# Performance work log

Hardware: AMD Instinct MI355X
Metric: run time of the kernel (lower is better)

## Reference

```python
import jax, jax.numpy as jnp
import numpy as np
from jax import lax

T, B, S = 64, 32, 64
V, E, H = 32000, 512, 512

def _p(key, shape, scale=0.05):
    return (jax.random.normal(key, shape, dtype=jnp.float32) * scale)

def setup_inputs() -> dict:
    key = jax.random.key(0)
    ks = jax.random.split(key, 24)
    inp = {
        'trg': jax.random.randint(ks[0], (T, B), 0, V),
        'encoded_src': jax.random.normal(ks[1], (S, B, 2 * H), dtype=jnp.float32),
        'emb': _p(ks[2], (V, E)),
        # LSTM layer 0: input = E + 2H
        'W_ih0': _p(ks[3], (4 * H, E + 2 * H)), 'W_hh0': _p(ks[4], (4 * H, H)),
        'b_ih0': _p(ks[5], (4 * H,)), 'b_hh0': _p(ks[6], (4 * H,)),
        # LSTM layer 1: input = H
        'W_ih1': _p(ks[7], (4 * H, H)), 'W_hh1': _p(ks[8], (4 * H, H)),
        'b_ih1': _p(ks[9], (4 * H,)), 'b_hh1': _p(ks[10], (4 * H,)),
        # attn_annot: 2H -> H
        'Wa': _p(ks[11], (H, 2 * H)), 'ba': _p(ks[12], (H,)),
        # attn_hidden: H -> H
        'Wh': _p(ks[13], (H, H)), 'bh': _p(ks[14], (H,)),
        # other: H -> 1
        'Wo': _p(ks[15], (1, H)), 'bo': _p(ks[16], (1,)),
        # penult: 3H -> E
        'Wp': _p(ks[17], (E, 3 * H)), 'bp': _p(ks[18], (E,)),
        # out bias (weight tied to emb)
        'b_out': _p(ks[19], (V,)),
    }
    return inp

def _lstm_cell(x, h, c, W_ih, W_hh, b_ih, b_hh):
    # PyTorch gate order: i, f, g, o
    g = x @ W_ih.T + b_ih + h @ W_hh.T + b_hh
    i, f, gg, o = jnp.split(g, 4, axis=-1)
    c_new = jax.nn.sigmoid(f) * c + jax.nn.sigmoid(i) * jnp.tanh(gg)
    h_new = jax.nn.sigmoid(o) * jnp.tanh(c_new)
    return h_new, c_new

def reference(trg, encoded_src, emb, W_ih0, W_hh0, b_ih0, b_hh0,
              W_ih1, W_hh1, b_ih1, b_hh1, Wa, ba, Wh, bh, Wo, bo,
              Wp, bp, b_out):
    trg_emb = emb[trg]                                # [T,B,E]
    annot_scores = encoded_src @ Wa.T + ba            # [S,B,H]
    Hd = W_hh0.shape[1]
    Bd = encoded_src.shape[1]
    h0 = jnp.zeros((2, Bd, Hd), dtype=encoded_src.dtype)
    c0 = jnp.zeros((2, Bd, Hd), dtype=encoded_src.dtype)
    ctx0 = jnp.zeros((Bd, encoded_src.shape[2]), dtype=encoded_src.dtype)

    def step(carry, emb_t):
        h, c, ctx = carry
        x = jnp.concatenate([emb_t, ctx], axis=1)      # [B, E+2H]
        h0n, c0n = _lstm_cell(x,   h[0], c[0], W_ih0, W_hh0, b_ih0, b_hh0)
        h1n, c1n = _lstm_cell(h0n, h[1], c[1], W_ih1, W_hh1, b_ih1, b_hh1)
        out = h1n                                      # [B,H]
        hs = out @ Wh.T + bh                           # [B,H]
        e = jnp.tanh(hs[None] + annot_scores) @ Wo.T + bo   # [S,B,1]
        a = jax.nn.softmax(e, axis=0)[..., 0]          # [S,B]
        ctx_new = jnp.einsum('sb,sbd->bd', a, encoded_src)  # [B,2H]
        stacked = jnp.concatenate([out, ctx_new], axis=1)   # [B,3H]
        return (jnp.stack([h0n, h1n]), jnp.stack([c0n, c1n]), ctx_new), stacked

    (h, c, _), all_scores = lax.scan(step, (h0, c0, ctx0), trg_emb)  # all_scores [T,B,3H]
    pen = all_scores @ Wp.T + bp                       # [T,B,E]
    logits = pen @ emb.T + b_out                       # [T,B,V] (tied weights)
    scores = jax.nn.log_softmax(logits, axis=2)
    return (scores, h, c)
```

## Files before the change

kernel.cpp:

```cpp
#include <hip/hip_runtime.h>


typedef unsigned short u16;
typedef short bf16x8 __attribute__((ext_vector_type(8)));
typedef float f32x4 __attribute__((ext_vector_type(4)));

#define MFMA_BF16(a, b, c) __builtin_amdgcn_mfma_f32_16x16x32_bf16((a), (b), (c), 0, 0, 0)

struct __attribute__((aligned(8))) U16x4 { u16 x, y, z, w; };

__device__ __forceinline__ float b2f(u16 u) {
  unsigned v = ((unsigned)u) << 16; float f; __builtin_memcpy(&f, &v, 4); return f;
}
__device__ __forceinline__ u16 f2b(float f) {
  unsigned u; __builtin_memcpy(&u, &f, 4);
  u = (u + 0x7FFFu + ((u >> 16) & 1u)) >> 16;
  return (u16)u;
}
__device__ __forceinline__ float sigm(float x) { return 1.f / (1.f + __expf(-x)); }
__device__ __forceinline__ float tanh_fast(float x) {
  x = fminf(fmaxf(x, -15.f), 15.f);
  float e = __expf(2.f * x);
  return (e - 1.f) / (e + 1.f);
}

__device__ __forceinline__ bf16x8 bl16(const u16* p) {
  bf16x8 v;
  asm volatile("global_load_dwordx4 %0, %1, off sc1" : "=v"(v) : "v"(p) : "memory");
  return v;
}
__device__ __forceinline__ float blf(const float* p) {
  float v;
  asm volatile("global_load_dword %0, %1, off sc1" : "=v"(v) : "v"(p) : "memory");
  return v;
}
__device__ __forceinline__ u16 blu16(const u16* p) {
  unsigned v;
  asm volatile("global_load_ushort %0, %1, off sc1" : "=v"(v) : "v"(p) : "memory");
  return (u16)v;
}
__device__ __forceinline__ void bs16(u16* p, u16 d) {
  unsigned dd = d;
  asm volatile("global_store_short %0, %1, off sc1" :: "v"(p), "v"(dd) : "memory");
}
__device__ __forceinline__ void bs32u(u16* p, unsigned d) {
  asm volatile("global_store_dword %0, %1, off sc1" :: "v"(p), "v"(d) : "memory");
}
__device__ __forceinline__ void bsf32(float* p, float d) {
  asm volatile("global_store_dword %0, %1, off sc1" :: "v"(p), "v"(d) : "memory");
}
__device__ __forceinline__ bf16x8 cl16(const u16* p) {
  bf16x8 v;
  asm volatile("global_load_dwordx4 %0, %1, off" : "=v"(v) : "v"(p));
  return v;
}
__device__ __forceinline__ void vmwait() {
  asm volatile("s_waitcnt vmcnt(0)" ::: "memory");
  __builtin_amdgcn_sched_barrier(0);
}

__device__ __forceinline__ void seg_f2b4(const float* src, u16* dst, long n4,
                                         int bid, int nb) {
  long i = (long)bid * 256 + threadIdx.x;
  long stride = (long)nb * 256;
  for (; i < n4; i += stride) {
    float4 v = ((const float4*)src)[i];
    U16x4 o; o.x = f2b(v.x); o.y = f2b(v.y); o.z = f2b(v.z); o.w = f2b(v.w);
    ((U16x4*)dst)[i] = o;
  }
}
__device__ __forceinline__ void seg_strided(const float* src, u16* dst,
                                            int rows, int cols4, int sld, int soff,
                                            int dld, int doff, int bid, int nb) {
  int total = rows * cols4;
  for (int i = bid * 256 + threadIdx.x; i < total; i += nb * 256) {
    int r = i / cols4, c4 = i - r * cols4;
    float4 v = *(const float4*)(src + (size_t)r * sld + soff + c4 * 4);
    U16x4 o; o.x = f2b(v.x); o.y = f2b(v.y); o.z = f2b(v.z); o.w = f2b(v.w);
    *(U16x4*)(dst + (size_t)r * dld + doff + c4 * 4) = o;
  }
}

__global__ __launch_bounds__(256) void prep_all(
    const float* __restrict__ emb, const float* __restrict__ enc,
    const float* __restrict__ Wa, const float* __restrict__ Wh,
    const float* __restrict__ Wp, const float* __restrict__ W_ih0,
    const float* __restrict__ W_hh0, const float* __restrict__ W_ih1,
    const float* __restrict__ W_hh1, const int* __restrict__ trg,
    u16* __restrict__ emb_b, u16* __restrict__ enc_b, u16* __restrict__ Wa_b,
    u16* __restrict__ Wh_b, u16* __restrict__ Wp_b, u16* __restrict__ Wemb0_b,
    u16* __restrict__ Wcat0_b, u16* __restrict__ Wcat1_b,
    u16* __restrict__ trgemb_b, u16* __restrict__ enc_bt,
    float* __restrict__ zero_base) {
  const int bx = blockIdx.x;
  if (bx < 32) {
    for (int i = bx * 256 + threadIdx.x; i < 24832; i += 32 * 256) {
      ((float4*)zero_base)[i] = make_float4(0.f, 0.f, 0.f, 0.f);
    }
  } else if (bx < 1056) {
    seg_f2b4(emb, emb_b, 4096000, bx - 32, 1024);
  } else if (bx < 1312) {
    seg_f2b4(enc, enc_b, 524288, bx - 1056, 256);
  } else if (bx < 1376) {
    seg_f2b4(Wa, Wa_b, 131072, bx - 1312, 64);
  } else if (bx < 1408) {
    seg_f2b4(Wh, Wh_b, 65536, bx - 1376, 32);
  } else if (bx < 1536) {
    seg_f2b4(Wp, Wp_b, 196608, bx - 1408, 128);
  } else if (bx < 2048) {
    seg_strided(W_ih0, Wemb0_b, 2048, 128, 1536, 0, 512, 0, bx - 1536, 512);
  } else if (bx < 2560) {
    seg_strided(W_ih0, Wcat0_b, 2048, 256, 1536, 512, 1536, 0, bx - 2048, 512);
  } else if (bx < 3072) {
    seg_strided(W_hh0, Wcat0_b, 2048, 128, 512, 0, 1536, 1024, bx - 2560, 512);
  } else if (bx < 3584) {
    seg_strided(W_ih1, Wcat1_b, 2048, 128, 512, 0, 1024, 0, bx - 3072, 512);
  } else if (bx < 4096) {
    seg_strided(W_hh1, Wcat1_b, 2048, 128, 512, 0, 1024, 512, bx - 3584, 512);
  } else if (bx < 6144) {
    int r = bx - 4096;
    int v = trg[r];
    const float* srow = emb + (size_t)v * 512;
    u16* drow = trgemb_b + (size_t)r * 512;
    for (int e = threadIdx.x; e < 128; e += 256) {
      float4 x = ((const float4*)srow)[e];
      U16x4 o; o.x = f2b(x.x); o.y = f2b(x.y); o.z = f2b(x.z); o.w = f2b(x.w);
      ((U16x4*)drow)[e] = o;
    }
  } else {
    int r = bx - 6144;
    int b = r >> 6, s = r & 63;
    const float* src = enc + (size_t)(s * 32 + b) * 1024;
    u16* dst = enc_bt + (size_t)(b * 64 + s) * 1024;
    int j = threadIdx.x;
    float4 v = ((const float4*)src)[j];
    U16x4 o; o.x = f2b(v.x); o.y = f2b(v.y); o.z = f2b(v.z); o.w = f2b(v.w);
    ((U16x4*)dst)[j] = o;
  }
}

template <int MODE>
__global__ __launch_bounds__(256) void gemm_bt(
    const u16* __restrict__ A, const u16* __restrict__ B,
    float* __restrict__ outF, u16* __restrict__ outB,
    const float* __restrict__ bias0, const float* __restrict__ bias1,
    int N, int K) {
  const int l = threadIdx.x & 63, wv = threadIdx.x >> 6;
  const int m0 = blockIdx.x * 128 + wv * 32;
  const int n0 = blockIdx.y * 64;
  const int kg = ((l >> 4) << 3);
  const u16* Ap0 = A + (size_t)(m0 + (l & 15)) * K + kg;
  const u16* Ap1 = Ap0 + (size_t)16 * K;
  const u16* Bp = B + (size_t)(n0 + (l & 15)) * K + kg;
  f32x4 acc[2][4] = {};
  for (int k0 = 0; k0 < K; k0 += 32) {
    bf16x8 a0 = *(const bf16x8*)(Ap0 + k0);
    bf16x8 a1 = *(const bf16x8*)(Ap1 + k0);
#pragma unroll
    for (int nf = 0; nf < 4; ++nf) {
      bf16x8 bb = *(const bf16x8*)(Bp + (size_t)(nf * 16) * K + k0);
      acc[0][nf] = MFMA_BF16(a0, bb, acc[0][nf]);
      acc[1][nf] = MFMA_BF16(a1, bb, acc[1][nf]);
    }
  }
  float biasv[4];
#pragma unroll
  for (int nf = 0; nf < 4; ++nf) {
    int col = n0 + nf * 16 + (l & 15);
    float bv = bias0 ? bias0[col] : 0.f;
    if (bias1) bv += bias1[col];
    biasv[nf] = bv;
  }
#pragma unroll
  for (int mi = 0; mi < 2; ++mi)
#pragma unroll
    for (int i = 0; i < 4; ++i) {
      int row = m0 + mi * 16 + ((l >> 4) << 2) + i;
#pragma unroll
      for (int nf = 0; nf < 4; ++nf) {
        int col = n0 + nf * 16 + (l & 15);
        float v = acc[mi][nf][i] + biasv[nf];
        if constexpr (MODE == 1) {
          outB[(size_t)row * N + col] = f2b(v);
        } else if constexpr (MODE == 3) {
          int b = row & 31, s = row >> 5;
          outB[(size_t)(b * 64 + s) * 512 + col] = f2b(v);
        } else {
          outF[(size_t)row * N + col] = v;
        }
      }
    }
}

__global__ __launch_bounds__(256) void logits_kernel(
    const u16* __restrict__ A,
    const u16* __restrict__ B,
    const float* __restrict__ bias,
    float* __restrict__ out,
    float* __restrict__ pmax, float* __restrict__ psum) {
  __shared__ float smf[128 * 132];
  const int id = blockIdx.x;
  const int lin = (id & 7) * 500 + (id >> 3);
  const int mt = lin & 15, nt = lin >> 4;
  const int gm = mt * 128, n0 = nt * 128;
  const int l = threadIdx.x & 63, wv = threadIdx.x >> 6;
  const int kg = ((l >> 4) << 3);
  const int m0 = gm + wv * 32;

  const u16* Ap0 = A + (size_t)(m0 + (l & 15)) * 512 + kg;
  const u16* Ap1 = Ap0 + (size_t)16 * 512;
  const u16* Bp = B + (size_t)(n0 + (l & 15)) * 512 + kg;
  f32x4 acc[2][8] = {};
  for (int k0 = 0; k0 < 512; k0 += 32) {
    bf16x8 a0 = *(const bf16x8*)(Ap0 + k0);
    bf16x8 a1 = *(const bf16x8*)(Ap1 + k0);
#pragma unroll
    for (int nf = 0; nf < 8; ++nf) {
      bf16x8 bb = *(const bf16x8*)(Bp + (size_t)(nf * 16) * 512 + k0);
      acc[0][nf] = MFMA_BF16(a0, bb, acc[0][nf]);
      acc[1][nf] = MFMA_BF16(a1, bb, acc[1][nf]);
    }
  }
  float bv[8];
#pragma unroll
  for (int nf = 0; nf < 8; ++nf) bv[nf] = bias[n0 + nf * 16 + (l & 15)];

  float lm[2][4], se[2][4];
#pragma unroll
  for (int mi = 0; mi < 2; ++mi)
#pragma unroll
    for (int i = 0; i < 4; ++i) {
      int rl = wv * 32 + mi * 16 + ((l >> 4) << 2) + i;
      float m_ = -3.4e38f;
#pragma unroll
      for (int nf = 0; nf < 8; ++nf) {
        float v = acc[mi][nf][i] + bv[nf];
        acc[mi][nf][i] = v;
        smf[rl * 132 + nf * 16 + (l & 15)] = v;
        m_ = fmaxf(m_, v);
      }
      lm[mi][i] = m_;
    }
#pragma unroll
  for (int d = 1; d < 16; d <<= 1)
#pragma unroll
    for (int mi = 0; mi < 2; ++mi)
#pragma unroll
      for (int i = 0; i < 4; ++i) lm[mi][i] = fmaxf(lm[mi][i], __shfl_xor(lm[mi][i], d));
#pragma unroll
  for (int mi = 0; mi < 2; ++mi)
#pragma unroll
    for (int i = 0; i < 4; ++i) {
      float s_ = 0.f;
#pragma unroll
      for (int nf = 0; nf < 8; ++nf) s_ += __expf(acc[mi][nf][i] - lm[mi][i]);
      se[mi][i] = s_;
    }
#pragma unroll
  for (int d = 1; d < 16; d <<= 1)
#pragma unroll
    for (int mi = 0; mi < 2; ++mi)
#pragma unroll
      for (int i = 0; i < 4; ++i) se[mi][i] += __shfl_xor(se[mi][i], d);
  if ((l & 15) == 0) {
#pragma unroll
    for (int mi = 0; mi < 2; ++mi)
#pragma unroll
      for (int i = 0; i < 4; ++i) {
        int row = m0 + mi * 16 + ((l >> 4) << 2) + i;
        pmax[(size_t)row * 250 + nt] = lm[mi][i];
        psum[(size_t)row * 250 + nt] = se[mi][i];
      }
  }
  __syncthreads();
#pragma unroll
  for (int r = 0; r < 128; r += 8) {
    int row = r + (threadIdx.x >> 5);
    int c4 = threadIdx.x & 31;
    float4 v = *(float4*)&smf[row * 132 + c4 * 4];
    *(float4*)&out[(size_t)(gm + row) * 32000 + n0 + c4 * 4] = v;
  }
}

__device__ __forceinline__ void grid_barrier(unsigned* flags, unsigned phase) {
  __syncthreads();
  if (threadIdx.x == 0) {
    __hip_atomic_store(flags + blockIdx.x * 32, phase, __ATOMIC_RELAXED,
                       __HIP_MEMORY_SCOPE_AGENT);
  }
  if (threadIdx.x < 32) {
    int spins = 0;
    while (__hip_atomic_load(flags + threadIdx.x * 32, __ATOMIC_RELAXED,
                             __HIP_MEMORY_SCOPE_AGENT) < phase &&
           spins < 2000000) ++spins;
  }
  __syncthreads();
}

__global__ __launch_bounds__(512, 2) void scan_kernel(
    const u16* __restrict__ xW0,
    const u16* __restrict__ Wcat0,
    const u16* __restrict__ Wcat1,
    const u16* __restrict__ Whb,
    const float* __restrict__ b_ih1, const float* __restrict__ b_hh1,
    const float* __restrict__ bh, const float* __restrict__ Wo, const float* __restrict__ bo,
    const u16* __restrict__ annot_bt,
    const u16* __restrict__ enc_bt,
    u16* __restrict__ ctxb,
    u16* __restrict__ h0b,
    u16* __restrict__ h1b,
    float* __restrict__ c0, float* __restrict__ c1,
    float* __restrict__ hs,
    u16* __restrict__ scoresb,
    float* __restrict__ dout_hc,
    unsigned* __restrict__ flags) {
  __shared__ float sm[16384];
  const int w = blockIdx.x;
  const int tid = threadIdx.x;
  const int l = tid & 63, wv = tid >> 6;
  const int jh0 = w * 16;
  const int bE = tid >> 4, jlE = tid & 15;
  unsigned phase = 0;

  float gb1[4];
#pragma unroll
  for (int g = 0; g < 4; ++g) gb1[g] = b_ih1[g * 512 + jh0 + jlE] + b_hh1[g * 512 + jh0 + jlE];
  const float bhv = bh[jh0 + jlE];
  const float bov = bo[0];

  for (int t = 0; t < 64; ++t) {
    const int pA = t & 1;
    {
      const int kg = ((l >> 4) << 3);
      u16 xw[4];
      {
        const u16* xp = xW0 + (size_t)(t * 32 + bE) * 2048 + jh0 + jlE;
#pragma unroll
        for (int g = 0; g < 4; ++g) xw[g] = blu16(xp + g * 512);
      }
      bf16x8 a0[6], a1[6];
#pragma unroll
      for (int kk = 0; kk < 6; ++kk) {
        const int k0 = wv * 192 + kk * 32;
        const u16* ab; int ld, off;
        if (k0 < 1024) { ab = ctxb; ld = 1024; off = k0; }
        else { ab = h0b + pA * 16384; ld = 512; off = k0 - 1024; }
        a0[kk] = bl16(ab + (size_t)(l & 15) * ld + off + kg);
        a1[kk] = bl16(ab + (size_t)((l & 15) + 16) * ld + off + kg);
      }
      vmwait();
      f32x4 acc[2][4] = {};
#pragma unroll
      for (int kk = 0; kk < 6; ++kk) {
        const int k0 = wv * 192 + kk * 32;
#pragma unroll
        for (int g = 0; g < 4; ++g) {
          bf16x8 bb = *(const bf16x8*)(Wcat0 + (size_t)(g * 512 + jh0 + (l & 15)) * 1536 + k0 + kg);
          acc[0][g] = MFMA_BF16(a0[kk], bb, acc[0][g]);
          acc[1][g] = MFMA_BF16(a1[kk], bb, acc[1][g]);
        }
      }
#pragma unroll
      for (int mi = 0; mi < 2; ++mi)
#pragma unroll
        for (int g = 0; g < 4; ++g)
#pragma unroll
          for (int i = 0; i < 4; ++i) {
            int m = mi * 16 + ((l >> 4) << 2) + i;
            sm[(wv * 32 + m) * 64 + g * 16 + (l & 15)] = acc[mi][g][i];
          }
      __syncthreads();
      {
        const int b = bE, jl = jlE, jh = jh0 + jl;
        float gate[4];
#pragma unroll
        for (int g = 0; g < 4; ++g) {
          float s = 0.f;
#pragma unroll
          for (int kv = 0; kv < 8; ++kv) s += sm[(kv * 32 + b) * 64 + g * 16 + jl];
          gate[g] = s + b2f(xw[g]);
        }
        float cn = sigm(gate[1]) * c0[b * 512 + jh] + sigm(gate[0]) * tanh_fast(gate[2]);
        float hn = sigm(gate[3]) * tanh_fast(cn);
        c0[b * 512 + jh] = cn;
        bs16(h0b + (pA ^ 1) * 16384 + b * 512 + jh, f2b(hn));
        if (t == 63) { dout_hc[b * 512 + jh] = hn; dout_hc[32768 + b * 512 + jh] = cn; }
      }
    }
    bf16x8 wB[16];
    {
      ++phase;
      __syncthreads();
      if (tid == 0)
        __hip_atomic_store(flags + blockIdx.x * 32, phase, __ATOMIC_RELAXED,
                           __HIP_MEMORY_SCOPE_AGENT);
      const int kg = ((l >> 4) << 3);
#pragma unroll
      for (int kk = 0; kk < 4; ++kk)
#pragma unroll
        for (int g = 0; g < 4; ++g)
          wB[kk * 4 + g] = cl16(Wcat1 + (size_t)(g * 512 + jh0 + (l & 15)) * 1024 +
                                wv * 128 + kk * 32 + kg);
      if (tid < 32) {
        int spins = 0;
        while (__hip_atomic_load(flags + tid * 32, __ATOMIC_RELAXED,
                                 __HIP_MEMORY_SCOPE_AGENT) < phase &&
               spins < 2000000) ++spins;
      }
      __syncthreads();
    }
    {
      const int kg = ((l >> 4) << 3);
      bf16x8 a0[4], a1[4];
#pragma unroll
      for (int kk = 0; kk < 4; ++kk) {
        const int k0 = wv * 128 + kk * 32;
        const u16* ab; int off;
        if (k0 < 512) { ab = h0b + (pA ^ 1) * 16384; off = k0; }
        else { ab = h1b + pA * 16384; off = k0 - 512; }
        a0[kk] = bl16(ab + (size_t)(l & 15) * 512 + off + kg);
        a1[kk] = bl16(ab + (size_t)((l & 15) + 16) * 512 + off + kg);
      }
      vmwait();
      f32x4 acc[2][4] = {};
#pragma unroll
      for (int kk = 0; kk < 4; ++kk) {
#pragma unroll
        for (int g = 0; g < 4; ++g) {
          acc[0][g] = MFMA_BF16(a0[kk], wB[kk * 4 + g], acc[0][g]);
          acc[1][g] = MFMA_BF16(a1[kk], wB[kk * 4 + g], acc[1][g]);
        }
      }
#pragma unroll
      for (int mi = 0; mi < 2; ++mi)
#pragma unroll
        for (int g = 0; g < 4; ++g)
#pragma unroll
          for (int i = 0; i < 4; ++i) {
            int m = mi * 16 + ((l >> 4) << 2) + i;
            sm[(wv * 32 + m) * 64 + g * 16 + (l & 15)] = acc[mi][g][i];
          }
      __syncthreads();
      {
        const int b = bE, jl = jlE, jh = jh0 + jl;
        float gate[4];
#pragma unroll
        for (int g = 0; g < 4; ++g) {
          float s = 0.f;
#pragma unroll
          for (int kv = 0; kv < 8; ++kv) s += sm[(kv * 32 + b) * 64 + g * 16 + jl];
          gate[g] = s + gb1[g];
        }
        float cn = sigm(gate[1]) * c1[b * 512 + jh] + sigm(gate[0]) * tanh_fast(gate[2]);
        float hn = sigm(gate[3]) * tanh_fast(cn);
        c1[b * 512 + jh] = cn;
        u16 hb = f2b(hn);
        bs16(h1b + (pA ^ 1) * 16384 + b * 512 + jh, hb);
        bs16(scoresb + (size_t)(t * 32 + b) * 1536 + jh, hb);
        if (t == 63) { dout_hc[16384 + b * 512 + jh] = hn; dout_hc[49152 + b * 512 + jh] = cn; }
      }
    }
    bf16x8 wC[2];
    {
      ++phase;
      __syncthreads();
      if (tid == 0)
        __hip_atomic_store(flags + blockIdx.x * 32, phase, __ATOMIC_RELAXED,
                           __HIP_MEMORY_SCOPE_AGENT);
      const int kg = ((l >> 4) << 3);
#pragma unroll
      for (int kk = 0; kk < 2; ++kk)
        wC[kk] = cl16(Whb + (size_t)(jh0 + (l & 15)) * 512 + wv * 64 + kk * 32 + kg);
      if (tid < 32) {
        int spins = 0;
        while (__hip_atomic_load(flags + tid * 32, __ATOMIC_RELAXED,
                                 __HIP_MEMORY_SCOPE_AGENT) < phase &&
               spins < 2000000) ++spins;
      }
      __syncthreads();
    }
    {
      const int kg = ((l >> 4) << 3);
      const u16* h1n = h1b + (pA ^ 1) * 16384;
      bf16x8 a0[2], a1[2];
#pragma unroll
      for (int kk = 0; kk < 2; ++kk) {
        const int k0 = wv * 64 + kk * 32;
        a0[kk] = bl16(h1n + (size_t)(l & 15) * 512 + k0 + kg);
        a1[kk] = bl16(h1n + (size_t)((l & 15) + 16) * 512 + k0 + kg);
      }
      vmwait();
      f32x4 acc2[2] = {};
#pragma unroll
      for (int kk = 0; kk < 2; ++kk) {
        acc2[0] = MFMA_BF16(a0[kk], wC[kk], acc2[0]);
        acc2[1] = MFMA_BF16(a1[kk], wC[kk], acc2[1]);
      }
#pragma unroll
      for (int mi = 0; mi < 2; ++mi)
#pragma unroll
        for (int i = 0; i < 4; ++i)
          sm[(wv * 32 + mi * 16 + ((l >> 4) << 2) + i) * 16 + (l & 15)] = acc2[mi][i];
      __syncthreads();
      {
        const int b = bE, jl = jlE;
        float s = 0.f;
#pragma unroll
        for (int kv = 0; kv < 8; ++kv) s += sm[(kv * 32 + b) * 16 + jl];
        bsf32(hs + b * 512 + jh0 + jl, s + bhv);
      }
    }
    grid_barrier(flags, ++phase);
    {
      const int b = w;
      float* hs_s = sm;
      float* wo_s = sm + 512;
      float* red = sm + 1024;
      float* a_s = sm + 1536;
      float hv = blf(hs + b * 512 + tid);
      float wov = Wo[tid];
      vmwait();
      hs_s[tid] = hv;
      wo_s[tid] = wov;
      __syncthreads();
      const int s_ = tid >> 3, ks = tid & 7;
      const u16* arow = annot_bt + (size_t)(b * 64 + s_) * 512 + ks * 64;
      float accv = 0.f;
#pragma unroll
      for (int kk8 = 0; kk8 < 8; ++kk8) {
        bf16x8 av = *(const bf16x8*)(arow + kk8 * 8);
#pragma unroll
        for (int j = 0; j < 8; ++j) {
          int k = ks * 64 + kk8 * 8 + j;
          accv += tanh_fast(hs_s[k] + b2f((u16)av[j])) * wo_s[k];
        }
      }
      red[tid] = accv;
      __syncthreads();
      if (tid < 64) {
        float e = bov;
#pragma unroll
        for (int j = 0; j < 8; ++j) e += red[tid * 8 + j];
        float mx = e;
#pragma unroll
        for (int d = 1; d < 64; d <<= 1) mx = fmaxf(mx, __shfl_xor(mx, d));
        float p = __expf(e - mx);
        float ss = p;
#pragma unroll
        for (int d = 1; d < 64; d <<= 1) ss += __shfl_xor(ss, d);
        a_s[tid] = p / ss;
      }
      __syncthreads();
      float cx0 = 0.f, cx1 = 0.f;
      const u16* erow = enc_bt + (size_t)b * 65536 + tid * 2;
#pragma unroll 8
      for (int s2 = 0; s2 < 64; ++s2) {
        unsigned ev = *(const unsigned*)(erow + (size_t)s2 * 1024);
        float av = a_s[s2];
        cx0 += av * b2f((u16)(ev & 0xFFFFu));
        cx1 += av * b2f((u16)(ev >> 16));
      }
      unsigned pk = (unsigned)f2b(cx0) | ((unsigned)f2b(cx1) << 16);
      bs32u(ctxb + b * 1024 + tid * 2, pk);
      bs32u(scoresb + (size_t)(t * 32 + b) * 1536 + 512 + tid * 2, pk);
    }
    grid_barrier(flags, ++phase);
  }
}

__global__ __launch_bounds__(256) void lse_kernel(const float* __restrict__ pmax,
                                                  const float* __restrict__ psum,
                                                  float* __restrict__ lse, int nt) {
  __shared__ float red[256];
  const int r = blockIdx.x;
  float m = -3.4e38f;
  for (int j = threadIdx.x; j < nt; j += 256) m = fmaxf(m, pmax[(size_t)r * nt + j]);
  red[threadIdx.x] = m; __syncthreads();
  for (int s = 128; s > 0; s >>= 1) {
    if (threadIdx.x < s) red[threadIdx.x] = fmaxf(red[threadIdx.x], red[threadIdx.x + s]);
    __syncthreads();
  }
  const float M = red[0]; __syncthreads();
  float s_ = 0.f;
  for (int j = threadIdx.x; j < nt; j += 256)
    s_ += psum[(size_t)r * nt + j] * __expf(pmax[(size_t)r * nt + j] - M);
  red[threadIdx.x] = s_; __syncthreads();
  for (int s = 128; s > 0; s >>= 1) {
    if (threadIdx.x < s) red[threadIdx.x] += red[threadIdx.x + s];
    __syncthreads();
  }
  if (threadIdx.x == 0) lse[r] = M + logf(red[0]);
}

__global__ void finalize_kernel(float* __restrict__ out, const float* __restrict__ lse) {
  const long n4 = 16384000;
  for (long i = (long)blockIdx.x * blockDim.x + threadIdx.x; i < n4;
       i += (long)gridDim.x * blockDim.x) {
    float4 v = ((float4*)out)[i];
    float L = lse[i / 8000];
    v.x -= L; v.y -= L; v.z -= L; v.w -= L;
    ((float4*)out)[i] = v;
  }
}

extern "C" void kernel_launch(void* const* d_in, const int* in_sizes, int n_in,
                              void* d_out, int out_size, void* d_ws, size_t ws_size,
                              hipStream_t stream) {
  const int* trg = (const int*)d_in[0];
  const float* enc = (const float*)d_in[1];
  const float* emb = (const float*)d_in[2];
  const float* W_ih0 = (const float*)d_in[3];
  const float* W_hh0 = (const float*)d_in[4];
  const float* b_ih0 = (const float*)d_in[5];
  const float* b_hh0 = (const float*)d_in[6];
  const float* W_ih1 = (const float*)d_in[7];
  const float* W_hh1 = (const float*)d_in[8];
  const float* b_ih1 = (const float*)d_in[9];
  const float* b_hh1 = (const float*)d_in[10];
  const float* Wa = (const float*)d_in[11];
  const float* ba = (const float*)d_in[12];
  const float* Wh = (const float*)d_in[13];
  const float* bh = (const float*)d_in[14];
  const float* Wo = (const float*)d_in[15];
  const float* bo = (const float*)d_in[16];
  const float* Wp = (const float*)d_in[17];
  const float* bp = (const float*)d_in[18];
  const float* b_out = (const float*)d_in[19];
  float* out = (float*)d_out;

  unsigned char* ws = (unsigned char*)d_ws;
  size_t off = 0;
  auto alloc = [&](size_t bytes) -> void* {
    void* p = ws + off; off += (bytes + 255) & ~(size_t)255; return p;
  };
  u16* emb_b = (u16*)alloc(32768000);
  u16* trgemb_b = (u16*)alloc(2097152);
  u16* enc_b = (u16*)alloc(4194304);
  u16* Wemb0_b = (u16*)alloc(2097152);
  u16* Wcat0_b = (u16*)alloc(6291456);
  u16* Wcat1_b = (u16*)alloc(4194304);
  u16* Wa_b = (u16*)alloc(1048576);
  u16* Wh_b = (u16*)alloc(524288);
  u16* Wp_b = (u16*)alloc(1572864);
  u16* xW0_b = (u16*)alloc(8388608);
  u16* scoresb = (u16*)alloc(6291456);
  u16* pen_b = (u16*)alloc(2097152);
  u16* ctxb = (u16*)alloc(65536);
  u16* h0b = (u16*)alloc(65536);
  u16* h1b = (u16*)alloc(65536);
  float* c0 = (float*)alloc(65536);
  float* c1 = (float*)alloc(65536);
  float* hsbuf = (float*)alloc(65536);
  unsigned* flags = (unsigned*)alloc(4096);
  float* pmax = (float*)alloc(4194304);
  float* psum = (float*)alloc(4194304);
  float* lse = (float*)alloc(8192);
  if (off > ws_size) return;

  u16* annot_bt = (u16*)pmax;
  u16* enc_bt = (u16*)psum;

  prep_all<<<8192, 256, 0, stream>>>(emb, enc, Wa, Wh, Wp, W_ih0, W_hh0, W_ih1, W_hh1,
                                     trg, emb_b, enc_b, Wa_b, Wh_b, Wp_b, Wemb0_b,
                                     Wcat0_b, Wcat1_b, trgemb_b, enc_bt, (float*)ctxb);

  gemm_bt<1><<<dim3(16, 32), 256, 0, stream>>>(trgemb_b, Wemb0_b, nullptr, xW0_b,
                                               b_ih0, b_hh0, 2048, 512);
  gemm_bt<3><<<dim3(16, 8), 256, 0, stream>>>(enc_b, Wa_b, nullptr, annot_bt,
                                              ba, nullptr, 512, 1024);

  scan_kernel<<<32, 512, 0, stream>>>(xW0_b, Wcat0_b, Wcat1_b, Wh_b, b_ih1, b_hh1, bh, Wo, bo,
                                      annot_bt, enc_bt, ctxb, h0b, h1b, c0, c1, hsbuf, scoresb,
                                      out + 65536000, flags);
  gemm_bt<1><<<dim3(16, 8), 256, 0, stream>>>(scoresb, Wp_b, nullptr, pen_b,
                                              bp, nullptr, 512, 1536);
  logits_kernel<<<4000, 256, 0, stream>>>(pen_b, emb_b, b_out, out, pmax, psum);
  lse_kernel<<<2048, 256, 0, stream>>>(pmax, psum, lse, 250);
  finalize_kernel<<<2048, 256, 0, stream>>>(out, lse);
}
```

Measured before the change: 2.361 ms.

## Hoist loop-invariant loads in scan, prefetch across barriers, fuse lse into finalize

```diff
diff --git a/kernel.cpp b/kernel.cpp
--- a/kernel.cpp
+++ b/kernel.cpp
@@ -282,21 +282,6 @@
   }
 }
 
-__device__ __forceinline__ void grid_barrier(unsigned* flags, unsigned phase) {
-  __syncthreads();
-  if (threadIdx.x == 0) {
-    __hip_atomic_store(flags + blockIdx.x * 32, phase, __ATOMIC_RELAXED,
-                       __HIP_MEMORY_SCOPE_AGENT);
-  }
-  if (threadIdx.x < 32) {
-    int spins = 0;
-    while (__hip_atomic_load(flags + threadIdx.x * 32, __ATOMIC_RELAXED,
-                             __HIP_MEMORY_SCOPE_AGENT) < phase &&
-           spins < 2000000) ++spins;
-  }
-  __syncthreads();
-}
-
 __global__ __launch_bounds__(512, 2) void scan_kernel(
     const u16* __restrict__ xW0,
     const u16* __restrict__ Wcat0,
@@ -320,6 +305,8 @@
   const int l = tid & 63, wv = tid >> 6;
   const int jh0 = w * 16;
   const int bE = tid >> 4, jlE = tid & 15;
+  const int kg = (l >> 4) << 3;
+  const int sA = tid >> 3, ksA = tid & 7;
   unsigned phase = 0;
 
   float gb1[4];
@@ -327,17 +314,30 @@
   for (int g = 0; g < 4; ++g) gb1[g] = b_ih1[g * 512 + jh0 + jlE] + b_hh1[g * 512 + jh0 + jlE];
   const float bhv = bh[jh0 + jlE];
   const float bov = bo[0];
+  const float wov = Wo[tid];
+
+  bf16x8 av_p[8];
+  {
+    const u16* arow = annot_bt + (size_t)(w * 64 + sA) * 512 + ksA * 64;
+#pragma unroll
+    for (int kk8 = 0; kk8 < 8; ++kk8) av_p[kk8] = cl16(arow + kk8 * 8);
+  }
+  bf16x8 wC[2];
+#pragma unroll
+  for (int kk = 0; kk < 2; ++kk)
+    wC[kk] = cl16(Whb + (size_t)(jh0 + (l & 15)) * 512 + wv * 64 + kk * 32 + kg);
+  const u16* erow = enc_bt + (size_t)w * 65536 + tid * 2;
+
+  u16 xw[4];
+  {
+    const u16* xp = xW0 + (size_t)(0 * 32 + bE) * 2048 + jh0 + jlE;
+#pragma unroll
+    for (int g = 0; g < 4; ++g) xw[g] = blu16(xp + g * 512);
+  }
 
   for (int t = 0; t < 64; ++t) {
     const int pA = t & 1;
     {
-      const int kg = ((l >> 4) << 3);
-      u16 xw[4];
-      {
-        const u16* xp = xW0 + (size_t)(t * 32 + bE) * 2048 + jh0 + jlE;
-#pragma unroll
-        for (int g = 0; g < 4; ++g) xw[g] = blu16(xp + g * 512);
-      }
       bf16x8 a0[6], a1[6];
 #pragma unroll
       for (int kk = 0; kk < 6; ++kk) {
@@ -394,7 +394,6 @@
       if (tid == 0)
         __hip_atomic_store(flags + blockIdx.x * 32, phase, __ATOMIC_RELAXED,
                            __HIP_MEMORY_SCOPE_AGENT);
-      const int kg = ((l >> 4) << 3);
 #pragma unroll
       for (int kk = 0; kk < 4; ++kk)
 #pragma unroll
@@ -410,7 +409,6 @@
       __syncthreads();
     }
     {
-      const int kg = ((l >> 4) << 3);
       bf16x8 a0[4], a1[4];
 #pragma unroll
       for (int kk = 0; kk < 4; ++kk) {
@@ -460,17 +458,16 @@
         if (t == 63) { dout_hc[16384 + b * 512 + jh] = hn; dout_hc[49152 + b * 512 + jh] = cn; }
       }
     }
-    bf16x8 wC[2];
+    unsigned encv[64];
     {
       ++phase;
       __syncthreads();
       if (tid == 0)
         __hip_atomic_store(flags + blockIdx.x * 32, phase, __ATOMIC_RELAXED,
                            __HIP_MEMORY_SCOPE_AGENT);
-      const int kg = ((l >> 4) << 3);
-#pragma unroll
-      for (int kk = 0; kk < 2; ++kk)
-        wC[kk] = cl16(Whb + (size_t)(jh0 + (l & 15)) * 512 + wv * 64 + kk * 32 + kg);
+#pragma unroll
+      for (int s2 = 0; s2 < 64; ++s2)
+        encv[s2] = *(const unsigned*)(erow + (size_t)s2 * 1024);
       if (tid < 32) {
         int spins = 0;
         while (__hip_atomic_load(flags + tid * 32, __ATOMIC_RELAXED,
@@ -480,7 +477,6 @@
       __syncthreads();
     }
     {
-      const int kg = ((l >> 4) << 3);
       const u16* h1n = h1b + (pA ^ 1) * 16384;
       bf16x8 a0[2], a1[2];
 #pragma unroll
@@ -510,7 +506,20 @@
         bsf32(hs + b * 512 + jh0 + jl, s + bhv);
       }
     }
-    grid_barrier(flags, ++phase);
+    {
+      ++phase;
+      __syncthreads();
+      if (tid == 0)
+        __hip_atomic_store(flags + blockIdx.x * 32, phase, __ATOMIC_RELAXED,
+                           __HIP_MEMORY_SCOPE_AGENT);
+      if (tid < 32) {
+        int spins = 0;
+        while (__hip_atomic_load(flags + tid * 32, __ATOMIC_RELAXED,
+                                 __HIP_MEMORY_SCOPE_AGENT) < phase &&
+               spins < 2000000) ++spins;
+      }
+      __syncthreads();
+    }
     {
       const int b = w;
       float* hs_s = sm;
@@ -518,20 +527,17 @@
       float* red = sm + 1024;
       float* a_s = sm + 1536;
       float hv = blf(hs + b * 512 + tid);
-      float wov = Wo[tid];
       vmwait();
       hs_s[tid] = hv;
       wo_s[tid] = wov;
       __syncthreads();
-      const int s_ = tid >> 3, ks = tid & 7;
-      const u16* arow = annot_bt + (size_t)(b * 64 + s_) * 512 + ks * 64;
       float accv = 0.f;
 #pragma unroll
       for (int kk8 = 0; kk8 < 8; ++kk8) {
-        bf16x8 av = *(const bf16x8*)(arow + kk8 * 8);
+        bf16x8 av = av_p[kk8];
 #pragma unroll
         for (int j = 0; j < 8; ++j) {
-          int k = ks * 64 + kk8 * 8 + j;
+          int k = ksA * 64 + kk8 * 8 + j;
           accv += tanh_fast(hs_s[k] + b2f((u16)av[j])) * wo_s[k];
         }
       }
@@ -552,10 +558,9 @@
       }
       __syncthreads();
       float cx0 = 0.f, cx1 = 0.f;
-      const u16* erow = enc_bt + (size_t)b * 65536 + tid * 2;
 #pragma unroll 8
       for (int s2 = 0; s2 < 64; ++s2) {
-        unsigned ev = *(const unsigned*)(erow + (size_t)s2 * 1024);
+        unsigned ev = encv[s2];
         float av = a_s[s2];
         cx0 += av * b2f((u16)(ev & 0xFFFFu));
         cx1 += av * b2f((u16)(ev >> 16));
@@ -564,42 +569,54 @@
       bs32u(ctxb + b * 1024 + tid * 2, pk);
       bs32u(scoresb + (size_t)(t * 32 + b) * 1536 + 512 + tid * 2, pk);
     }
-    grid_barrier(flags, ++phase);
-  }
-}
-
-__global__ __launch_bounds__(256) void lse_kernel(const float* __restrict__ pmax,
-                                                  const float* __restrict__ psum,
-                                                  float* __restrict__ lse, int nt) {
+    {
+      ++phase;
+      __syncthreads();
+      if (tid == 0)
+        __hip_atomic_store(flags + blockIdx.x * 32, phase, __ATOMIC_RELAXED,
+                           __HIP_MEMORY_SCOPE_AGENT);
+      {
+        const int tn = (t + 1) & 63;
+        const u16* xp = xW0 + (size_t)(tn * 32 + bE) * 2048 + jh0 + jlE;
+#pragma unroll
+        for (int g = 0; g < 4; ++g) xw[g] = blu16(xp + g * 512);
+      }
+      if (tid < 32) {
+        int spins = 0;
+        while (__hip_atomic_load(flags + tid * 32, __ATOMIC_RELAXED,
+                                 __HIP_MEMORY_SCOPE_AGENT) < phase &&
+               spins < 2000000) ++spins;
+      }
+      __syncthreads();
+    }
+  }
+}
+
+__global__ __launch_bounds__(256) void lsefin_kernel(const float* __restrict__ pmax,
+                                                     const float* __restrict__ psum,
+                                                     float* __restrict__ out) {
   __shared__ float red[256];
   const int r = blockIdx.x;
-  float m = -3.4e38f;
-  for (int j = threadIdx.x; j < nt; j += 256) m = fmaxf(m, pmax[(size_t)r * nt + j]);
-  red[threadIdx.x] = m; __syncthreads();
+  const int tid = threadIdx.x;
+  float pm = (tid < 250) ? pmax[(size_t)r * 250 + tid] : -3.4e38f;
+  float ps = (tid < 250) ? psum[(size_t)r * 250 + tid] : 0.f;
+  red[tid] = pm; __syncthreads();
   for (int s = 128; s > 0; s >>= 1) {
-    if (threadIdx.x < s) red[threadIdx.x] = fmaxf(red[threadIdx.x], red[threadIdx.x + s]);
+    if (tid < s) red[tid] = fmaxf(red[tid], red[tid + s]);
     __syncthreads();
   }
   const float M = red[0]; __syncthreads();
-  float s_ = 0.f;
-  for (int j = threadIdx.x; j < nt; j += 256)
-    s_ += psum[(size_t)r * nt + j] * __expf(pmax[(size_t)r * nt + j] - M);
-  red[threadIdx.x] = s_; __syncthreads();
+  red[tid] = ps * __expf(pm - M); __syncthreads();
   for (int s = 128; s > 0; s >>= 1) {
-    if (threadIdx.x < s) red[threadIdx.x] += red[threadIdx.x + s];
+    if (tid < s) red[tid] += red[tid + s];
     __syncthreads();
   }
-  if (threadIdx.x == 0) lse[r] = M + logf(red[0]);
-}
-
-__global__ void finalize_kernel(float* __restrict__ out, const float* __restrict__ lse) {
-  const long n4 = 16384000;
-  for (long i = (long)blockIdx.x * blockDim.x + threadIdx.x; i < n4;
-       i += (long)gridDim.x * blockDim.x) {
-    float4 v = ((float4*)out)[i];
-    float L = lse[i / 8000];
+  const float L = M + logf(red[0]);
+  float4* rowp = (float4*)(out + (size_t)r * 32000);
+  for (int i = tid; i < 8000; i += 256) {
+    float4 v = rowp[i];
     v.x -= L; v.y -= L; v.z -= L; v.w -= L;
-    ((float4*)out)[i] = v;
+    rowp[i] = v;
   }
 }
 
@@ -654,7 +671,6 @@
   unsigned* flags = (unsigned*)alloc(4096);
   float* pmax = (float*)alloc(4194304);
   float* psum = (float*)alloc(4194304);
-  float* lse = (float*)alloc(8192);
   if (off > ws_size) return;
 
   u16* annot_bt = (u16*)pmax;
@@ -675,6 +691,5 @@
   gemm_bt<1><<<dim3(16, 8), 256, 0, stream>>>(scoresb, Wp_b, nullptr, pen_b,
                                               bp, nullptr, 512, 1536);
   logits_kernel<<<4000, 256, 0, stream>>>(pen_b, emb_b, b_out, out, pmax, psum);
-  lse_kernel<<<2048, 256, 0, stream>>>(pmax, psum, lse, 250);
-  finalize_kernel<<<2048, 256, 0, stream>>>(out, lse);
-}
+  lsefin_kernel<<<2048, 256, 0, stream>>>(pmax, psum, out);
+}
```

Result: slower. 4.339 ms (+83.7%).
